# Kernel tuning notes

Hardware: AMD Instinct MI355X
Metric: run time of the kernel (lower is better)

The kernel has to match this reference:

```python
import jax, jax.numpy as jnp
import numpy as np

CODE_DIMS = [256, 512, 1024, 2048]
C = 256
BETA = 0.25
B = 64
N = 1024


def setup_inputs() -> dict:
    key = jax.random.key(0)
    ks = jax.random.split(key, 2 + len(CODE_DIMS))
    z_e = jax.random.normal(ks[0], (B, N, C), dtype=jnp.float32)
    expert_idx = jax.random.randint(ks[1], (B,), 0, len(CODE_DIMS))
    s = 1.0 / np.sqrt(C)  # torch uniform init bound
    inp = {"z_e": z_e, "expert_idx": expert_idx}
    for r, K in enumerate(CODE_DIMS):
        inp[f"cb{r}"] = jax.random.uniform(ks[2 + r], (K, C), minval=-s, maxval=s, dtype=jnp.float32)
    return inp


def _vq_expert(z_e, cb):
    # z_e: [B, N, C], cb: [K, C]
    Bz, Nz, Cz = z_e.shape
    zf = z_e.reshape(-1, Cz)                                  # [B*N, C]
    dists = ((zf ** 2).sum(axis=1, keepdims=True)
             + (cb ** 2).sum(axis=1)[None, :]
             - 2.0 * zf @ cb.T)                               # [B*N, K]
    idx = jnp.argmin(dists, axis=1)                           # [B*N]
    z_q = cb[idx].reshape(Bz, Nz, Cz)                         # [B, N, C]
    return z_q, idx.reshape(Bz, Nz)


def reference(z_e, expert_idx, cb0, cb1, cb2, cb3):
    cbs = [cb0, cb1, cb2, cb3]
    Bz, Nz, Cz = z_e.shape
    sg = jax.lax.stop_gradient
    z_q_out = jnp.zeros_like(z_e)
    indices = jnp.zeros((Bz, Nz), dtype=jnp.int32)
    vq_loss = jnp.asarray(0.0, dtype=z_e.dtype)
    for r, cb in enumerate(cbs):
        z_q, idx = _vq_expert(z_e, cb)
        mask = expert_idx == r                                # [B]
        mf = mask.astype(z_e.dtype)[:, None, None]            # [B,1,1]
        cnt = mask.sum().astype(z_e.dtype)
        denom = jnp.maximum(cnt * Nz * Cz, 1.0)               # mean over masked subset
        codebook_loss = jnp.sum(mf * (sg(z_q) - z_e) ** 2) / denom
        commit_loss = jnp.sum(mf * (z_q - sg(z_e)) ** 2) / denom
        loss_r = (codebook_loss + BETA * commit_loss) / Cz
        frac = cnt / Bz                                       # z_in.numel()/z_e.numel()
        vq_loss = vq_loss + frac * loss_r
        z_q_st = z_e + sg(z_q - z_e)                          # straight-through
        z_q_out = jnp.where(mf > 0, z_q_st, z_q_out)
        indices = jnp.where(mask[:, None], idx.astype(jnp.int32), indices)
    return z_q_out, indices, vq_loss
```

## Files before the change

kernel.cpp:

```cpp
#include <hip/hip_runtime.h>
#include <hip/hip_bf16.h>


#define EPS_GAP 2e-3f
#define NTOK 65536

typedef __attribute__((ext_vector_type(8))) short bf16x8;
typedef __attribute__((ext_vector_type(4))) float f32x4;

__device__ inline unsigned short f2bf(float f) {
  __hip_bfloat16 h = __float2bfloat16(f);
  unsigned short u;
  __builtin_memcpy(&u, &h, 2);
  return u;
}
__device__ inline float bf2f(unsigned short u) {
  return __uint_as_float(((unsigned)u) << 16);
}

__device__ inline void gll16(const unsigned short* g, unsigned short* l) {
  __builtin_amdgcn_global_load_lds(
      (const __attribute__((address_space(1))) unsigned int*)g,
      (__attribute__((address_space(3))) unsigned int*)l, 16, 0, 0);
}

__global__ __launch_bounds__(256) void csum_split_kernel(
    const float* __restrict__ cb0, const float* __restrict__ cb1,
    const float* __restrict__ cb2, const float* __restrict__ cb3,
    float* __restrict__ csums, double* __restrict__ csums64,
    unsigned short* __restrict__ cb_hi, unsigned short* __restrict__ cb_lo,
    int* __restrict__ wl_cnt) {
  if (blockIdx.x == 0 && threadIdx.x == 0) wl_cnt[0] = 0;
  int row = blockIdx.x * 4 + (threadIdx.x >> 6);
  int lane = threadIdx.x & 63;
  const float* src; int r;
  if (row < 256)       { src = cb0; r = row; }
  else if (row < 768)  { src = cb1; r = row - 256; }
  else if (row < 1792) { src = cb2; r = row - 768; }
  else                 { src = cb3; r = row - 1792; }
  float4 v = ((const float4*)(src + r * 256))[lane];
  unsigned short h0 = f2bf(v.x), h1 = f2bf(v.y), h2 = f2bf(v.z), h3 = f2bf(v.w);
  unsigned short l0 = f2bf(v.x - bf2f(h0)), l1 = f2bf(v.y - bf2f(h1));
  unsigned short l2 = f2bf(v.z - bf2f(h2)), l3 = f2bf(v.w - bf2f(h3));
  *(ushort4*)(cb_hi + (size_t)row * 256 + lane * 4) = make_ushort4(h0, h1, h2, h3);
  *(ushort4*)(cb_lo + (size_t)row * 256 + lane * 4) = make_ushort4(l0, l1, l2, l3);
  double s = (double)v.x*v.x + (double)v.y*v.y + (double)v.z*v.z + (double)v.w*v.w;
  #pragma unroll
  for (int off = 32; off >= 1; off >>= 1) s += __shfl_down(s, off, 64);
  if (lane == 0) { csums[row] = (float)s; csums64[row] = s; }
}

__global__ __launch_bounds__(256) void ze_split_kernel(
    const float* __restrict__ z, unsigned short* __restrict__ ze_hi,
    unsigned short* __restrict__ ze_lo, double* __restrict__ parts) {
  const float4* p = (const float4*)z;
  uint2* hi = (uint2*)ze_hi;
  uint2* lo = (uint2*)ze_lo;
  const int n4 = 4194304;
  double s = 0.0;
  for (int i = blockIdx.x * 256 + threadIdx.x; i < n4; i += 256 * 1024) {
    float4 v = p[i];
    unsigned hxy, hzw, lxy, lzw;
    asm("v_cvt_pk_bf16_f32 %0, %1, %2" : "=v"(hxy) : "v"(v.x), "v"(v.y));
    asm("v_cvt_pk_bf16_f32 %0, %1, %2" : "=v"(hzw) : "v"(v.z), "v"(v.w));
    float lx = v.x - __uint_as_float(hxy << 16);
    float ly = v.y - __uint_as_float(hxy & 0xffff0000u);
    float lz = v.z - __uint_as_float(hzw << 16);
    float lw = v.w - __uint_as_float(hzw & 0xffff0000u);
    asm("v_cvt_pk_bf16_f32 %0, %1, %2" : "=v"(lxy) : "v"(lx), "v"(ly));
    asm("v_cvt_pk_bf16_f32 %0, %1, %2" : "=v"(lzw) : "v"(lz), "v"(lw));
    hi[i] = make_uint2(hxy, hzw);
    lo[i] = make_uint2(lxy, lzw);
    s += (double)v.x*(double)v.x + (double)v.y*(double)v.y
       + (double)v.z*(double)v.z + (double)v.w*(double)v.w;
  }
  #pragma unroll
  for (int off = 32; off >= 1; off >>= 1) s += __shfl_down(s, off, 64);
  __shared__ double sh[4];
  if ((threadIdx.x & 63) == 0) sh[threadIdx.x >> 6] = s;
  __syncthreads();
  if (threadIdx.x == 0) parts[blockIdx.x] = sh[0] + sh[1] + sh[2] + sh[3];
}

__global__ __launch_bounds__(512, 4) void vq_mfma(
    const unsigned short* __restrict__ ze_hi, const unsigned short* __restrict__ ze_lo,
    const int* __restrict__ expert_idx,
    const unsigned short* __restrict__ cb_hi, const unsigned short* __restrict__ cb_lo,
    const float* __restrict__ csums,
    float* __restrict__ D1, int* __restrict__ K1, float* __restrict__ D2) {
  const int b  = blockIdx.y;
  const int e  = expert_idx[b];
  const int hc = blockIdx.z;
  if (hc >= (2 << e)) return;
  const int cs_off = (e == 0) ? 0 : (e == 1) ? 256 : (e == 2) ? 768 : 1792;
  const int krow0  = cs_off + hc * 128;
  const int t0     = b * 1024 + blockIdx.x * 128;

  __shared__ unsigned short smem[2 * 4 * 128 * 32];
  __shared__ float  sh_cs[128];

  const int tid = threadIdx.x;
  if (tid < 128) sh_cs[tid] = csums[krow0 + tid];

  const int w = tid >> 6, l = tid & 63;
  const int h = w >> 2, q = w & 3;
  const int m16 = l & 15, g = l >> 4;

  const int srow   = w * 16 + (l >> 2);
  const int schunk = (l & 3) ^ ((srow >> 1) & 3);
  const size_t asrc = (size_t)(t0 + srow) * 256 + (size_t)schunk * 8;
  const size_t bsrc = (size_t)(krow0 + srow) * 256 + (size_t)schunk * 8;
  const int wslot = w * 512;

  f32x4 acc[4][2];
  #pragma unroll
  for (int i = 0; i < 4; ++i)
    #pragma unroll
    for (int j = 0; j < 2; ++j) acc[i][j] = (f32x4){0.f, 0.f, 0.f, 0.f};

  gll16(ze_hi + asrc, smem + wslot);
  gll16(ze_lo + asrc, smem + 4096 + wslot);
  gll16(cb_hi + bsrc, smem + 8192 + wslot);
  gll16(cb_lo + bsrc, smem + 12288 + wslot);

  for (int kp = 0; kp < 8; ++kp) {
    unsigned short* buf = smem + (kp & 1) * 16384;
    if (kp < 7) {
      const int kcn = (kp + 1) * 32;
      unsigned short* nb = smem + ((kp & 1) ^ 1) * 16384;
      gll16(ze_hi + asrc + kcn, nb + wslot);
      gll16(ze_lo + asrc + kcn, nb + 4096 + wslot);
      gll16(cb_hi + bsrc + kcn, nb + 8192 + wslot);
      gll16(cb_lo + bsrc + kcn, nb + 12288 + wslot);
      asm volatile("s_waitcnt vmcnt(4)" ::: "memory");
    } else {
      asm volatile("s_waitcnt vmcnt(0)" ::: "memory");
    }
    __builtin_amdgcn_s_barrier();

    unsigned short* Ah = buf;
    unsigned short* Al = buf + 4096;
    unsigned short* Bh = buf + 8192;
    unsigned short* Bl = buf + 12288;
    bf16x8 bh[2], bl[2];
    #pragma unroll
    for (int j = 0; j < 2; ++j) {
      int r = q * 32 + j * 16 + m16;
      int n = r * 32 + ((g ^ ((r >> 1) & 3)) << 3);
      bh[j] = *(bf16x8*)(Bh + n);
      bl[j] = *(bf16x8*)(Bl + n);
    }
    #pragma unroll
    for (int i = 0; i < 4; ++i) {
      int r = h * 64 + i * 16 + m16;
      int a = r * 32 + ((g ^ ((r >> 1) & 3)) << 3);
      bf16x8 ah = *(bf16x8*)(Ah + a);
      bf16x8 al = *(bf16x8*)(Al + a);
      #pragma unroll
      for (int j = 0; j < 2; ++j) {
        acc[i][j] = __builtin_amdgcn_mfma_f32_16x16x32_bf16(ah, bh[j], acc[i][j], 0, 0, 0);
        acc[i][j] = __builtin_amdgcn_mfma_f32_16x16x32_bf16(al, bh[j], acc[i][j], 0, 0, 0);
        acc[i][j] = __builtin_amdgcn_mfma_f32_16x16x32_bf16(ah, bl[j], acc[i][j], 0, 0, 0);
      }
    }
    __builtin_amdgcn_sched_barrier(0);
    __builtin_amdgcn_s_barrier();
  }

  __syncthreads();
  float* mD = (float*)smem;
  int*   mK = (int*)(smem + 1024);
  float* mS = (float*)(smem + 2048);

  #pragma unroll
  for (int i = 0; i < 4; ++i) {
    #pragma unroll
    for (int r = 0; r < 4; ++r) {
      int k0 = q * 32 + m16;
      float d0 = sh_cs[k0]      - 2.0f * acc[i][0][r];
      float d1 = sh_cs[k0 + 16] - 2.0f * acc[i][1][r];
      float bv, sv; int bk;
      if (d0 <= d1) { bv = d0; bk = k0; sv = d1; }
      else          { bv = d1; bk = k0 + 16; sv = d0; }
      #pragma unroll
      for (int off = 8; off >= 1; off >>= 1) {
        float ov = __shfl_xor(bv, off);
        int   ok = __shfl_xor(bk, off);
        float os = __shfl_xor(sv, off);
        float nb; int nk;
        if (ov < bv || (ov == bv && ok < bk)) { nb = ov; nk = ok; }
        else                                  { nb = bv; nk = bk; }
        sv = fminf(fmaxf(bv, ov), fminf(sv, os));
        bv = nb; bk = nk;
      }
      if (m16 == 0) {
        int tloc = h * 64 + i * 16 + g * 4 + r;
        mD[tloc * 4 + q] = bv;
        mK[tloc * 4 + q] = bk;
        mS[tloc * 4 + q] = sv;
      }
    }
  }
  __syncthreads();
  if (tid < 128) {
    float B = 3.4e38f, S = 3.4e38f; int Kb = 0;
    #pragma unroll
    for (int c = 0; c < 4; ++c) {
      float d1v = mD[tid * 4 + c];
      int   k1v = mK[tid * 4 + c];
      float d2v = mS[tid * 4 + c];
      S = fminf(fmaxf(B, d1v), fminf(S, d2v));
      if (d1v < B) { B = d1v; Kb = k1v; }
    }
    int tg = t0 + tid;
    D1[hc * NTOK + tg] = B;
    K1[hc * NTOK + tg] = hc * 128 + Kb;
    D2[hc * NTOK + tg] = S;
  }
}

__global__ __launch_bounds__(256) void combine_kernel(
    const int* __restrict__ expert_idx,
    const float* __restrict__ D1, const int* __restrict__ K1,
    const float* __restrict__ D2,
    float* __restrict__ idx_out,
    int* __restrict__ wl, int* __restrict__ wl_cnt,
    double* __restrict__ parts) {
  const int t = blockIdx.x * 256 + threadIdx.x;
  const int e = expert_idx[t >> 10];
  const int nch = 2 << e;
  float B = 3.4e38f, S = 3.4e38f; int Kb = 0;
  for (int c = 0; c < nch; ++c) {
    float d1 = D1[c * NTOK + t];
    int   k1 = K1[c * NTOK + t];
    float d2 = D2[c * NTOK + t];
    S = fminf(fmaxf(B, d1), fminf(S, d2));
    if (d1 < B) { B = d1; Kb = k1; }
  }
  idx_out[t] = (float)Kb;
  if (S - B < EPS_GAP) {
    int p = atomicAdd(wl_cnt, 1);
    wl[p] = t;
  }
  double s = (double)B;
  #pragma unroll
  for (int off = 32; off >= 1; off >>= 1) s += __shfl_down(s, off, 64);
  __shared__ double sh[4];
  if ((threadIdx.x & 63) == 0) sh[threadIdx.x >> 6] = s;
  __syncthreads();
  if (threadIdx.x == 0) parts[blockIdx.x] = sh[0] + sh[1] + sh[2] + sh[3];
}

__global__ __launch_bounds__(256) void zq_gather_kernel(
    const int* __restrict__ expert_idx,
    const float* __restrict__ cb0, const float* __restrict__ cb1,
    const float* __restrict__ cb2, const float* __restrict__ cb3,
    const float* __restrict__ idx_out, float* __restrict__ zq_out) {
  const int tok  = blockIdx.x * 4 + (threadIdx.x >> 6);
  const int lane = threadIdx.x & 63;
  const int e = expert_idx[tok >> 10];
  const float* cb = (e == 0) ? cb0 : (e == 1) ? cb1 : (e == 2) ? cb2 : cb3;
  const int row = (int)idx_out[tok];
  ((float4*)(zq_out + (size_t)tok * 256))[lane] =
      ((const float4*)(cb + (size_t)row * 256))[lane];
}

__global__ __launch_bounds__(256) void rescue_kernel(
    const float* __restrict__ z_e, const int* __restrict__ expert_idx,
    const float* __restrict__ cb0, const float* __restrict__ cb1,
    const float* __restrict__ cb2, const float* __restrict__ cb3,
    const double* __restrict__ csums64,
    const int* __restrict__ wl, const int* __restrict__ wl_cnt,
    float* __restrict__ zq_out, float* __restrict__ idx_out) {
  __shared__ float  szrow[256];
  __shared__ double szs[4];
  __shared__ float  sdv[3][256];
  __shared__ int    skv[3][256];
  __shared__ int    s_kc;
  const int tid = threadIdx.x;
  const int wid = tid >> 6, lane = tid & 63;
  const int n = wl_cnt[0];
  for (int it = blockIdx.x; it < n; it += gridDim.x) {
    const int t = wl[it];
    const int b = t >> 10;
    const int e = expert_idx[b];
    const int K = 256 << e;
    const float* cb = (e == 0) ? cb0 : (e == 1) ? cb1 : (e == 2) ? cb2 : cb3;
    const int off = (e == 0) ? 0 : (e == 1) ? 256 : (e == 2) ? 768 : 1792;
    const double* cs64 = csums64 + off;

    __syncthreads();
    float zv = z_e[(size_t)t * 256 + tid];
    szrow[tid] = zv;
    double zsq = (double)zv * (double)zv;
    #pragma unroll
    for (int o = 32; o >= 1; o >>= 1) zsq += __shfl_down(zsq, o, 64);
    if (lane == 0) szs[wid] = zsq;
    __syncthreads();
    const float zs_mid = (float)(szs[0] + szs[1] + szs[2] + szs[3]);
    const unsigned zu = __float_as_uint(zs_mid);
    float zs[3] = {__uint_as_float(zu - 1), zs_mid, __uint_as_float(zu + 1)};

    float bd[3] = {3.4e38f, 3.4e38f, 3.4e38f};
    int   bk[3] = {1 << 30, 1 << 30, 1 << 30};
    const float4* z4 = (const float4*)szrow;
    for (int k = tid; k < K; k += 256) {
      const float4* c4 = (const float4*)(cb + (size_t)k * 256);
      double d0 = 0.0, d1v = 0.0, d2v = 0.0, d3 = 0.0;
      for (int qq = 0; qq < 64; qq += 4) {
        float4 a0 = z4[qq],     c0 = c4[qq];
        float4 a1 = z4[qq + 1], c1 = c4[qq + 1];
        float4 a2 = z4[qq + 2], c2 = c4[qq + 2];
        float4 a3 = z4[qq + 3], c3 = c4[qq + 3];
        d0 += (double)a0.x*c0.x + (double)a0.y*c0.y + (double)a0.z*c0.z + (double)a0.w*c0.w;
        d1v+= (double)a1.x*c1.x + (double)a1.y*c1.y + (double)a1.z*c1.z + (double)a1.w*c1.w;
        d2v+= (double)a2.x*c2.x + (double)a2.y*c2.y + (double)a2.z*c2.z + (double)a2.w*c2.w;
        d3 += (double)a3.x*c3.x + (double)a3.y*c3.y + (double)a3.z*c3.z + (double)a3.w*c3.w;
      }
      double dot = (d0 + d1v) + (d2v + d3);
      const float c32 = (float)cs64[k];
      const float m2d = (float)(2.0 * dot);
      #pragma unroll
      for (int v = 0; v < 3; ++v) {
        float T1  = zs[v] + c32;
        float d32 = T1 - m2d;
        if (d32 < bd[v]) { bd[v] = d32; bk[v] = k; }
      }
    }
    #pragma unroll
    for (int v = 0; v < 3; ++v) { sdv[v][tid] = bd[v]; skv[v][tid] = bk[v]; }
    __syncthreads();
    for (int s = 128; s >= 1; s >>= 1) {
      if (tid < s) {
        #pragma unroll
        for (int v = 0; v < 3; ++v) {
          float od = sdv[v][tid + s]; int ok = skv[v][tid + s];
          if (od < sdv[v][tid] || (od == sdv[v][tid] && ok < skv[v][tid])) {
            sdv[v][tid] = od; skv[v][tid] = ok;
          }
        }
      }
      __syncthreads();
    }
    if (tid == 0) {
      int k0 = skv[0][0], k1 = skv[1][0], k2 = skv[2][0];
      int kc = (k0 == k2) ? k0 : k1;
      s_kc = kc;
      idx_out[t] = (float)kc;
    }
    __syncthreads();
    const int kc = s_kc;
    if (tid < 64)
      ((float4*)(zq_out + (size_t)t * 256))[tid] =
          ((const float4*)(cb + (size_t)kc * 256))[tid];
  }
}

__global__ __launch_bounds__(256) void finalize_kernel(
    const double* __restrict__ parts_comb, const double* __restrict__ parts_zsq,
    float* __restrict__ loss_out) {
  const int tid = threadIdx.x;
  double s = parts_comb[tid] + parts_zsq[tid] + parts_zsq[tid + 256]
           + parts_zsq[tid + 512] + parts_zsq[tid + 768];
  #pragma unroll
  for (int off = 32; off >= 1; off >>= 1) s += __shfl_down(s, off, 64);
  __shared__ double sh[4];
  if ((tid & 63) == 0) sh[tid >> 6] = s;
  __syncthreads();
  if (tid == 0)
    loss_out[0] = (float)((sh[0] + sh[1] + sh[2] + sh[3]) * (1.25 / 4294967296.0));
}

extern "C" void kernel_launch(void* const* d_in, const int* in_sizes, int n_in,
                              void* d_out, int out_size, void* d_ws, size_t ws_size,
                              hipStream_t stream) {
  const float* z_e  = (const float*)d_in[0];
  const int*   eidx = (const int*)d_in[1];
  const float* cb0  = (const float*)d_in[2];
  const float* cb1  = (const float*)d_in[3];
  const float* cb2  = (const float*)d_in[4];
  const float* cb3  = (const float*)d_in[5];

  float* zq    = (float*)d_out;
  float* idxf  = (float*)d_out + 16777216;
  float* lossf = (float*)d_out + 16777216 + 65536;

  unsigned short* ze_hi = (unsigned short*)d_out;
  unsigned short* ze_lo = ze_hi + 16777216;

  char* wsp = (char*)d_ws;
  double*         parts_comb = (double*)wsp;           wsp += 256 * 8;
  double*         parts_zsq  = (double*)wsp;           wsp += 1024 * 8;
  double*         csums64    = (double*)wsp;           wsp += 3840 * 8;
  float*          csums      = (float*)wsp;            wsp += 3840 * 4;
  int*            wl_cnt     = (int*)wsp;              wsp += 16;
  int*            wl         = (int*)wsp;              wsp += NTOK * 4;
  unsigned short* cb_hi      = (unsigned short*)wsp;   wsp += 3840 * 256 * 2;
  unsigned short* cb_lo      = (unsigned short*)wsp;   wsp += 3840 * 256 * 2;
  float*          D1         = (float*)wsp;            wsp += 16 * NTOK * 4;
  int*            K1         = (int*)wsp;              wsp += 16 * NTOK * 4;
  float*          D2         = (float*)wsp;            wsp += 16 * NTOK * 4;

  csum_split_kernel<<<960, 256, 0, stream>>>(cb0, cb1, cb2, cb3,
                                             csums, csums64, cb_hi, cb_lo, wl_cnt);
  ze_split_kernel<<<1024, 256, 0, stream>>>(z_e, ze_hi, ze_lo, parts_zsq);
  dim3 grid(8, 64, 16);
  vq_mfma<<<grid, 512, 0, stream>>>(ze_hi, ze_lo, eidx, cb_hi, cb_lo, csums, D1, K1, D2);
  combine_kernel<<<256, 256, 0, stream>>>(eidx, D1, K1, D2, idxf, wl, wl_cnt, parts_comb);
  zq_gather_kernel<<<16384, 256, 0, stream>>>(eidx, cb0, cb1, cb2, cb3, idxf, zq);
  rescue_kernel<<<2048, 256, 0, stream>>>(z_e, eidx, cb0, cb1, cb2, cb3,
                                          csums64, wl, wl_cnt, zq, idxf);
  finalize_kernel<<<1, 256, 0, stream>>>(parts_comb, parts_zsq, lossf);
}
```

Measured before the change: 399.5 us.

## Load z_e fragments directly to registers, halve LDS, fuse gather into combine

The MFMA distance kernel now stages only codebook tiles in LDS and loads the z_e hi/lo fragments straight from global memory into registers. This halves shared memory per block and raises the occupancy hint from 4 to 6. The wave layout changes to 2x4 tiles so the argmin is mostly done within each lane, with fewer cross-lane shuffles. The separate z_q gather kernel is folded into combine_kernel, which removes one launch and the re-read of the index array. The cost is uncoalesced direct global loads for the A operand, and a gather that now runs on only 256 blocks.

```diff
diff --git a/kernel.cpp b/kernel.cpp
--- a/kernel.cpp
+++ b/kernel.cpp
@@ -82,7 +82,7 @@
   if (threadIdx.x == 0) parts[blockIdx.x] = sh[0] + sh[1] + sh[2] + sh[3];
 }
 
-__global__ __launch_bounds__(512, 4) void vq_mfma(
+__global__ __launch_bounds__(512, 6) void vq_mfma(
     const unsigned short* __restrict__ ze_hi, const unsigned short* __restrict__ ze_lo,
     const int* __restrict__ expert_idx,
     const unsigned short* __restrict__ cb_hi, const unsigned short* __restrict__ cb_lo,
@@ -96,72 +96,62 @@
   const int krow0  = cs_off + hc * 128;
   const int t0     = b * 1024 + blockIdx.x * 128;
 
-  __shared__ unsigned short smem[2 * 4 * 128 * 32];
-  __shared__ float  sh_cs[128];
+  __shared__ unsigned short smem[2 * 2 * 128 * 32];
+  __shared__ float sh_cs[128];
 
   const int tid = threadIdx.x;
   if (tid < 128) sh_cs[tid] = csums[krow0 + tid];
 
   const int w = tid >> 6, l = tid & 63;
-  const int h = w >> 2, q = w & 3;
+  const int h = w >> 1, q = w & 1;
   const int m16 = l & 15, g = l >> 4;
 
   const int srow   = w * 16 + (l >> 2);
   const int schunk = (l & 3) ^ ((srow >> 1) & 3);
-  const size_t asrc = (size_t)(t0 + srow) * 256 + (size_t)schunk * 8;
   const size_t bsrc = (size_t)(krow0 + srow) * 256 + (size_t)schunk * 8;
   const int wslot = w * 512;
 
-  f32x4 acc[4][2];
-  #pragma unroll
-  for (int i = 0; i < 4; ++i)
-    #pragma unroll
-    for (int j = 0; j < 2; ++j) acc[i][j] = (f32x4){0.f, 0.f, 0.f, 0.f};
-
-  gll16(ze_hi + asrc, smem + wslot);
-  gll16(ze_lo + asrc, smem + 4096 + wslot);
-  gll16(cb_hi + bsrc, smem + 8192 + wslot);
-  gll16(cb_lo + bsrc, smem + 12288 + wslot);
+  const size_t a0 = (size_t)(t0 + h * 32 + m16) * 256 + (size_t)g * 8;
+  const size_t a1 = a0 + 16 * 256;
+
+  f32x4 acc[2][4];
+  #pragma unroll
+  for (int i = 0; i < 2; ++i)
+    #pragma unroll
+    for (int j = 0; j < 4; ++j) acc[i][j] = (f32x4){0.f, 0.f, 0.f, 0.f};
+
+  gll16(cb_hi + bsrc, smem + wslot);
+  gll16(cb_lo + bsrc, smem + 4096 + wslot);
 
   for (int kp = 0; kp < 8; ++kp) {
-    unsigned short* buf = smem + (kp & 1) * 16384;
+    const int kc = kp * 32;
+    unsigned short* buf = smem + (kp & 1) * 8192;
+    bf16x8 ah0 = *(const bf16x8*)(ze_hi + a0 + kc);
+    bf16x8 al0 = *(const bf16x8*)(ze_lo + a0 + kc);
+    bf16x8 ah1 = *(const bf16x8*)(ze_hi + a1 + kc);
+    bf16x8 al1 = *(const bf16x8*)(ze_lo + a1 + kc);
     if (kp < 7) {
-      const int kcn = (kp + 1) * 32;
-      unsigned short* nb = smem + ((kp & 1) ^ 1) * 16384;
-      gll16(ze_hi + asrc + kcn, nb + wslot);
-      gll16(ze_lo + asrc + kcn, nb + 4096 + wslot);
-      gll16(cb_hi + bsrc + kcn, nb + 8192 + wslot);
-      gll16(cb_lo + bsrc + kcn, nb + 12288 + wslot);
-      asm volatile("s_waitcnt vmcnt(4)" ::: "memory");
+      unsigned short* nb = smem + ((kp & 1) ^ 1) * 8192;
+      gll16(cb_hi + bsrc + kc + 32, nb + wslot);
+      gll16(cb_lo + bsrc + kc + 32, nb + 4096 + wslot);
+      asm volatile("s_waitcnt vmcnt(2)" ::: "memory");
     } else {
       asm volatile("s_waitcnt vmcnt(0)" ::: "memory");
     }
     __builtin_amdgcn_s_barrier();
 
-    unsigned short* Ah = buf;
-    unsigned short* Al = buf + 4096;
-    unsigned short* Bh = buf + 8192;
-    unsigned short* Bl = buf + 12288;
-    bf16x8 bh[2], bl[2];
-    #pragma unroll
-    for (int j = 0; j < 2; ++j) {
-      int r = q * 32 + j * 16 + m16;
-      int n = r * 32 + ((g ^ ((r >> 1) & 3)) << 3);
-      bh[j] = *(bf16x8*)(Bh + n);
-      bl[j] = *(bf16x8*)(Bl + n);
-    }
-    #pragma unroll
-    for (int i = 0; i < 4; ++i) {
-      int r = h * 64 + i * 16 + m16;
-      int a = r * 32 + ((g ^ ((r >> 1) & 3)) << 3);
-      bf16x8 ah = *(bf16x8*)(Ah + a);
-      bf16x8 al = *(bf16x8*)(Al + a);
-      #pragma unroll
-      for (int j = 0; j < 2; ++j) {
-        acc[i][j] = __builtin_amdgcn_mfma_f32_16x16x32_bf16(ah, bh[j], acc[i][j], 0, 0, 0);
-        acc[i][j] = __builtin_amdgcn_mfma_f32_16x16x32_bf16(al, bh[j], acc[i][j], 0, 0, 0);
-        acc[i][j] = __builtin_amdgcn_mfma_f32_16x16x32_bf16(ah, bl[j], acc[i][j], 0, 0, 0);
-      }
+    #pragma unroll
+    for (int j = 0; j < 4; ++j) {
+      int row = q * 64 + j * 16 + m16;
+      int n = row * 32 + ((g ^ ((row >> 1) & 3)) << 3);
+      bf16x8 bh = *(bf16x8*)(buf + n);
+      bf16x8 bl = *(bf16x8*)(buf + 4096 + n);
+      acc[0][j] = __builtin_amdgcn_mfma_f32_16x16x32_bf16(bh, ah0, acc[0][j], 0, 0, 0);
+      acc[0][j] = __builtin_amdgcn_mfma_f32_16x16x32_bf16(bl, ah0, acc[0][j], 0, 0, 0);
+      acc[0][j] = __builtin_amdgcn_mfma_f32_16x16x32_bf16(bh, al0, acc[0][j], 0, 0, 0);
+      acc[1][j] = __builtin_amdgcn_mfma_f32_16x16x32_bf16(bh, ah1, acc[1][j], 0, 0, 0);
+      acc[1][j] = __builtin_amdgcn_mfma_f32_16x16x32_bf16(bl, ah1, acc[1][j], 0, 0, 0);
+      acc[1][j] = __builtin_amdgcn_mfma_f32_16x16x32_bf16(bh, al1, acc[1][j], 0, 0, 0);
     }
     __builtin_amdgcn_sched_barrier(0);
     __builtin_amdgcn_s_barrier();
@@ -169,46 +159,55 @@
 
   __syncthreads();
   float* mD = (float*)smem;
-  int*   mK = (int*)(smem + 1024);
-  float* mS = (float*)(smem + 2048);
-
-  #pragma unroll
-  for (int i = 0; i < 4; ++i) {
-    #pragma unroll
-    for (int r = 0; r < 4; ++r) {
-      int k0 = q * 32 + m16;
-      float d0 = sh_cs[k0]      - 2.0f * acc[i][0][r];
-      float d1 = sh_cs[k0 + 16] - 2.0f * acc[i][1][r];
-      float bv, sv; int bk;
-      if (d0 <= d1) { bv = d0; bk = k0; sv = d1; }
-      else          { bv = d1; bk = k0 + 16; sv = d0; }
+  int*   mK = (int*)(smem + 512);
+  float* mS = (float*)(smem + 1024);
+
+  float cst[16];
+  #pragma unroll
+  for (int j = 0; j < 4; ++j)
+    #pragma unroll
+    for (int r = 0; r < 4; ++r)
+      cst[j * 4 + r] = sh_cs[q * 64 + j * 16 + g * 4 + r];
+
+  #pragma unroll
+  for (int i = 0; i < 2; ++i) {
+    float bv = 3.4e38f, sv = 3.4e38f; int bk = 0;
+    #pragma unroll
+    for (int j = 0; j < 4; ++j) {
       #pragma unroll
-      for (int off = 8; off >= 1; off >>= 1) {
-        float ov = __shfl_xor(bv, off);
-        int   ok = __shfl_xor(bk, off);
-        float os = __shfl_xor(sv, off);
-        float nb; int nk;
-        if (ov < bv || (ov == bv && ok < bk)) { nb = ov; nk = ok; }
-        else                                  { nb = bv; nk = bk; }
-        sv = fminf(fmaxf(bv, ov), fminf(sv, os));
-        bv = nb; bk = nk;
+      for (int r = 0; r < 4; ++r) {
+        float d = fmaf(-2.0f, acc[i][j][r], cst[j * 4 + r]);
+        int   c = q * 64 + j * 16 + g * 4 + r;
+        if (d < bv) { sv = bv; bv = d; bk = c; }
+        else        { sv = fminf(sv, d); }
       }
-      if (m16 == 0) {
-        int tloc = h * 64 + i * 16 + g * 4 + r;
-        mD[tloc * 4 + q] = bv;
-        mK[tloc * 4 + q] = bk;
-        mS[tloc * 4 + q] = sv;
-      }
+    }
+    #pragma unroll
+    for (int off = 16; off <= 32; off <<= 1) {
+      float ov = __shfl_xor(bv, off);
+      int   ok = __shfl_xor(bk, off);
+      float os = __shfl_xor(sv, off);
+      float nb; int nk;
+      if (ov < bv || (ov == bv && ok < bk)) { nb = ov; nk = ok; }
+      else                                  { nb = bv; nk = bk; }
+      sv = fminf(fmaxf(bv, ov), fminf(sv, os));
+      bv = nb; bk = nk;
+    }
+    if (g == 0) {
+      int tloc = h * 32 + i * 16 + m16;
+      mD[tloc * 2 + q] = bv;
+      mK[tloc * 2 + q] = bk;
+      mS[tloc * 2 + q] = sv;
     }
   }
   __syncthreads();
   if (tid < 128) {
     float B = 3.4e38f, S = 3.4e38f; int Kb = 0;
     #pragma unroll
-    for (int c = 0; c < 4; ++c) {
-      float d1v = mD[tid * 4 + c];
-      int   k1v = mK[tid * 4 + c];
-      float d2v = mS[tid * 4 + c];
+    for (int c = 0; c < 2; ++c) {
+      float d1v = mD[tid * 2 + c];
+      int   k1v = mK[tid * 2 + c];
+      float d2v = mS[tid * 2 + c];
       S = fminf(fmaxf(B, d1v), fminf(S, d2v));
       if (d1v < B) { B = d1v; Kb = k1v; }
     }
@@ -223,11 +222,16 @@
     const int* __restrict__ expert_idx,
     const float* __restrict__ D1, const int* __restrict__ K1,
     const float* __restrict__ D2,
+    const float* __restrict__ cb0, const float* __restrict__ cb1,
+    const float* __restrict__ cb2, const float* __restrict__ cb3,
     float* __restrict__ idx_out,
     int* __restrict__ wl, int* __restrict__ wl_cnt,
-    double* __restrict__ parts) {
-  const int t = blockIdx.x * 256 + threadIdx.x;
-  const int e = expert_idx[t >> 10];
+    double* __restrict__ parts, float* __restrict__ zq_out) {
+  __shared__ int sh_idx[256];
+  __shared__ double shp[4];
+  const int bid = blockIdx.x;
+  const int t = bid * 256 + threadIdx.x;
+  const int e = expert_idx[bid >> 2];
   const int nch = 2 << e;
   float B = 3.4e38f, S = 3.4e38f; int Kb = 0;
   for (int c = 0; c < nch; ++c) {
@@ -238,6 +242,7 @@
     if (d1 < B) { B = d1; Kb = k1; }
   }
   idx_out[t] = (float)Kb;
+  sh_idx[threadIdx.x] = Kb;
   if (S - B < EPS_GAP) {
     int p = atomicAdd(wl_cnt, 1);
     wl[p] = t;
@@ -245,24 +250,18 @@
   double s = (double)B;
   #pragma unroll
   for (int off = 32; off >= 1; off >>= 1) s += __shfl_down(s, off, 64);
-  __shared__ double sh[4];
-  if ((threadIdx.x & 63) == 0) sh[threadIdx.x >> 6] = s;
+  if ((threadIdx.x & 63) == 0) shp[threadIdx.x >> 6] = s;
   __syncthreads();
-  if (threadIdx.x == 0) parts[blockIdx.x] = sh[0] + sh[1] + sh[2] + sh[3];
-}
-
-__global__ __launch_bounds__(256) void zq_gather_kernel(
-    const int* __restrict__ expert_idx,
-    const float* __restrict__ cb0, const float* __restrict__ cb1,
-    const float* __restrict__ cb2, const float* __restrict__ cb3,
-    const float* __restrict__ idx_out, float* __restrict__ zq_out) {
-  const int tok  = blockIdx.x * 4 + (threadIdx.x >> 6);
-  const int lane = threadIdx.x & 63;
-  const int e = expert_idx[tok >> 10];
+  if (threadIdx.x == 0) parts[bid] = shp[0] + shp[1] + shp[2] + shp[3];
+
   const float* cb = (e == 0) ? cb0 : (e == 1) ? cb1 : (e == 2) ? cb2 : cb3;
-  const int row = (int)idx_out[tok];
-  ((float4*)(zq_out + (size_t)tok * 256))[lane] =
-      ((const float4*)(cb + (size_t)row * 256))[lane];
+  const int wid = threadIdx.x >> 6, lane = threadIdx.x & 63;
+  for (int it = 0; it < 64; ++it) {
+    int tl = it * 4 + wid;
+    int row = sh_idx[tl];
+    ((float4*)(zq_out + (size_t)(bid * 256 + tl) * 256))[lane] =
+        ((const float4*)(cb + (size_t)row * 256))[lane];
+  }
 }
 
 __global__ __launch_bounds__(256) void rescue_kernel(
@@ -406,8 +405,8 @@
   ze_split_kernel<<<1024, 256, 0, stream>>>(z_e, ze_hi, ze_lo, parts_zsq);
   dim3 grid(8, 64, 16);
   vq_mfma<<<grid, 512, 0, stream>>>(ze_hi, ze_lo, eidx, cb_hi, cb_lo, csums, D1, K1, D2);
-  combine_kernel<<<256, 256, 0, stream>>>(eidx, D1, K1, D2, idxf, wl, wl_cnt, parts_comb);
-  zq_gather_kernel<<<16384, 256, 0, stream>>>(eidx, cb0, cb1, cb2, cb3, idxf, zq);
+  combine_kernel<<<256, 256, 0, stream>>>(eidx, D1, K1, D2, cb0, cb1, cb2, cb3,
+                                          idxf, wl, wl_cnt, parts_comb, zq);
   rescue_kernel<<<2048, 256, 0, stream>>>(z_e, eidx, cb0, cb1, cb2, cb3,
                                           csums64, wl, wl_cnt, zq, idxf);
   finalize_kernel<<<1, 256, 0, stream>>>(parts_comb, parts_zsq, lossf);
```

Result: no change. 403.8 us (+1.1%).
